# Kernel tuning notes

Measured on AMD Instinct MI355X. Metric: run time of the kernel, lower is better.

## Reference

```python
import jax, jax.numpy as jnp
import numpy as np

B, T, C, H = 128, 256, 384, 6
D = C // H  # head dim = 64


def setup_inputs() -> dict:
    key = jax.random.key(0)
    k1, k2, k3, k4, k5 = jax.random.split(key, 5)
    s = 0.02
    return {
        "x": jax.random.normal(k1, (B, T, C), dtype=jnp.float32),
        "W_qkv": jax.random.normal(k2, (C, 3 * C), dtype=jnp.float32) * s,
        "b_qkv": jax.random.normal(k3, (3 * C,), dtype=jnp.float32) * s,
        "W_proj": jax.random.normal(k4, (C, C), dtype=jnp.float32) * s,
        "b_proj": jax.random.normal(k5, (C,), dtype=jnp.float32) * s,
    }


def reference(x, W_qkv, b_qkv, W_proj, b_proj):
    Bv, Tv, Cv = x.shape
    # fused QKV projection, then split
    qkv = x @ W_qkv + b_qkv                      # [B,T,3C]
    q, k, v = jnp.split(qkv, 3, axis=-1)
    # [B,T,C] -> [B,H,T,D]
    q = q.reshape(Bv, Tv, H, D).transpose(0, 2, 1, 3)
    k = k.reshape(Bv, Tv, H, D).transpose(0, 2, 1, 3)
    v = v.reshape(Bv, Tv, H, D).transpose(0, 2, 1, 3)
    # causal masked scores, scaled by head_dim**-0.5
    scores = jnp.einsum("bhqd,bhkd->bhqk", q, k) * (D ** -0.5)
    causal = jnp.tril(jnp.ones((Tv, Tv), dtype=bool))
    scores = jnp.where(causal, scores, -jnp.inf)
    wt = jax.nn.softmax(scores, axis=-1)
    # dropout layers are identity in eval mode
    out = jnp.einsum("bhqk,bhkd->bhqd", wt, v)   # [B,H,T,D]
    out = out.transpose(0, 2, 1, 3).reshape(Bv, Tv, Cv)
    return out @ W_proj + b_proj
```

## Files before the change

### kernel.cpp

```cpp
#include <hip/hip_runtime.h>

typedef unsigned short u16;
typedef unsigned int u32;
typedef __attribute__((ext_vector_type(4))) float f32x4;
typedef __attribute__((ext_vector_type(8))) __bf16 bf16x8;
typedef __attribute__((ext_vector_type(2))) __bf16 bf16x2;

#define NEGINF (-1e30f)
#define QSCALE 0.18033688011112042f

__device__ __forceinline__ u16 f32_to_bf16(float f) {
  union { float f; unsigned int u; } v;
  v.f = f;
  unsigned int u = v.u;
  u += 0x7fffu + ((u >> 16) & 1u);
  return (u16)(u >> 16);
}

__device__ __forceinline__ u32 pk_bf16(float a, float b) {
  bf16x2 t;
  t.x = (__bf16)a;
  t.y = (__bf16)b;
  return __builtin_bit_cast(u32, t);
}

__device__ __forceinline__ f32x4 mfma_bf16(bf16x8 a, bf16x8 b, f32x4 c) {
  return __builtin_amdgcn_mfma_f32_16x16x32_bf16(a, b, c, 0, 0, 0);
}

#define GLOAD_LDS16(g, l) __builtin_amdgcn_global_load_lds( \
    (const __attribute__((address_space(1))) unsigned int*)(g), \
    (__attribute__((address_space(3))) unsigned int*)(l), 16, 0, 0)

__global__ void k_cvt4(const float4* __restrict__ in, u16* __restrict__ out, int nq) {
  int i = blockIdx.x * blockDim.x + threadIdx.x;
  if (i >= nq) return;
  float4 v = in[i];
  uint2 o;
  o.x = (unsigned int)f32_to_bf16(v.x) | ((unsigned int)f32_to_bf16(v.y) << 16);
  o.y = (unsigned int)f32_to_bf16(v.z) | ((unsigned int)f32_to_bf16(v.w) << 16);
  *(uint2*)(out + (size_t)i * 4) = o;
}

__global__ void k_tcvt(const float* __restrict__ in, u16* __restrict__ out, int K, int N) {
  int idx = blockIdx.x * blockDim.x + threadIdx.x;
  if (idx >= K * N) return;
  int k = idx / N, n = idx - k * N;
  out[(size_t)n * K + k] = f32_to_bf16(in[idx]);
}

__device__ __forceinline__ void gemm256x64(
    const u16* __restrict__ A, const u16* __restrict__ Bt,
    int mBase, int nBase, u16* lsA, u16* lsB,
    f32x4 acc[4][2], int lane, int wv, int wm, int wn) {
  const int l15 = lane & 15;
  size_t aoff[4];
  u32 aldso[4];
#pragma unroll
  for (int jj = 0; jj < 4; ++jj) {
    int c = wv * 256 + jj * 64 + lane;
    int row = c >> 3;
    int kc = (c & 7) ^ (row & 7);
    aoff[jj] = (size_t)(mBase + row) * 384 + kc * 8;
    aldso[jj] = (u32)(wv * 256 + jj * 64) * 8;
  }
  int cb = wv * 64 + lane;
  int brow = cb >> 3;
  size_t boff = (size_t)(nBase + brow) * 384 + (size_t)(((cb & 7) ^ (brow & 7)) * 8);
  u32 bldso = (u32)(wv * 64) * 8;

#define STAGE_T(kt, buf) do { \
  _Pragma("unroll") \
  for (int jj = 0; jj < 4; ++jj) \
    GLOAD_LDS16(A + aoff[jj] + (kt), lsA + (buf) * 16384 + aldso[jj]); \
  GLOAD_LDS16(Bt + boff + (kt), lsB + (buf) * 4096 + bldso); \
  } while (0)

  STAGE_T(0, 0);
#pragma unroll
  for (int t = 0; t < 6; ++t) {
    const int cur = t & 1;
    if (t < 5) {
      STAGE_T((t + 1) * 64, cur ^ 1);
      asm volatile("s_waitcnt vmcnt(5)" ::: "memory");
    } else {
      asm volatile("s_waitcnt vmcnt(0)" ::: "memory");
    }
    __builtin_amdgcn_s_barrier();
    const char* bA = (const char*)(lsA + cur * 16384);
    const char* bB = (const char*)(lsB + cur * 4096);
#pragma unroll
    for (int ks = 0; ks < 2; ++ks) {
      bf16x8 af[4], bfr[2];
#pragma unroll
      for (int i = 0; i < 4; ++i) {
        int row = wm * 64 + i * 16 + l15;
        af[i] = *(const bf16x8*)(bA + row * 128 + (((ks * 4 + (lane >> 4)) ^ (row & 7)) << 4));
      }
#pragma unroll
      for (int j = 0; j < 2; ++j) {
        int row = wn * 32 + j * 16 + l15;
        bfr[j] = *(const bf16x8*)(bB + row * 128 + (((ks * 4 + (lane >> 4)) ^ (row & 7)) << 4));
      }
#pragma unroll
      for (int i = 0; i < 4; ++i)
#pragma unroll
        for (int j = 0; j < 2; ++j)
          acc[i][j] = mfma_bf16(af[i], bfr[j], acc[i][j]);
    }
    __builtin_amdgcn_s_barrier();
  }
#undef STAGE_T
}

__global__ __launch_bounds__(512, 4) void k_qkv(
    const u16* __restrict__ A, const u16* __restrict__ Bt,
    const float* __restrict__ bias,
    u16* __restrict__ Qb, u16* __restrict__ Kb, u16* __restrict__ Vtb) {
  __shared__ __align__(16) u16 lsA[2 * 16384];
  __shared__ __align__(16) u16 lsB[2 * 4096];
  const int tid = threadIdx.x, lane = tid & 63, wv = tid >> 6;
  const int l15 = lane & 15, g = lane >> 4;
  const int wm = wv >> 1, wn = wv & 1;
  const int bid = (int)blockIdx.x;
  const int wgid = (bid & 7) * 288 + (bid >> 3);
  const int mtile = wgid / 18, ntile = wgid % 18;
  const int mBase = mtile * 256, nBase = ntile * 64;
  f32x4 acc[4][2] = {};
  gemm256x64(A, Bt, mBase, nBase, lsA, lsB, acc, lane, wv, wm, wn);

  const int part = nBase / 384;
  const int cbase = nBase - part * 384;
#pragma unroll
  for (int j = 0; j < 2; ++j) {
    int c = cbase + wn * 32 + j * 16 + l15;
    float bv = bias[nBase + wn * 32 + j * 16 + l15];
    int hh = c >> 6, d = c & 63;
    size_t bhh = (size_t)(mtile * 6 + hh);
#pragma unroll
    for (int i = 0; i < 4; ++i) {
      int t0 = wm * 64 + i * 16 + g * 4;
      if (part == 2) {
        uint2 w;
        w.x = pk_bf16(acc[i][j][0] + bv, acc[i][j][1] + bv);
        w.y = pk_bf16(acc[i][j][2] + bv, acc[i][j][3] + bv);
        *(uint2*)(Vtb + (bhh * 64 + d) * 256 + t0) = w;
      } else if (part == 0) {
#pragma unroll
        for (int r = 0; r < 4; ++r)
          Qb[(bhh * 256 + t0 + r) * 64 + d] = f32_to_bf16((acc[i][j][r] + bv) * QSCALE);
      } else {
#pragma unroll
        for (int r = 0; r < 4; ++r)
          Kb[(bhh * 256 + t0 + r) * 64 + d] = f32_to_bf16(acc[i][j][r] + bv);
      }
    }
  }
}

__global__ __launch_bounds__(64, 3) void k_attn(
    const u16* __restrict__ Qb, const u16* __restrict__ Kb,
    const u16* __restrict__ Vtb, u16* __restrict__ Ob) {
  __shared__ __align__(16) u16 lsP[32 * 64];
  const int lane = threadIdx.x;
  const int l15 = lane & 15, g = lane >> 4;
  const int s = 7 - (int)blockIdx.y;
  const int bh = blockIdx.x;
  const int b = bh / 6, h = bh % 6;
  const u16* Qh = Qb + (size_t)bh * (256 * 64);
  const u16* Kh = Kb + (size_t)bh * (256 * 64);
  const u16* Vh = Vtb + (size_t)bh * (64 * 256);
  const int ktiles = (s >> 1) + 1;
  char* pbuf = (char*)lsP;

  bf16x8 qf[2][2];
#pragma unroll
  for (int ks = 0; ks < 2; ++ks)
#pragma unroll
    for (int iq = 0; iq < 2; ++iq)
      qf[ks][iq] = *(const bf16x8*)(Qh + (size_t)(s * 32 + iq * 16 + l15) * 64 + ks * 32 + g * 8);

  f32x4 o[4][2] = {};
  float rl[2] = {0.f, 0.f};

#pragma unroll 1
  for (int kt = 0; kt < ktiles; ++kt) {
    bf16x8 kf[2][4];
#pragma unroll
    for (int ks = 0; ks < 2; ++ks)
#pragma unroll
      for (int jk = 0; jk < 4; ++jk)
        kf[ks][jk] = *(const bf16x8*)(Kh + (size_t)(kt * 64 + jk * 16 + l15) * 64 + ks * 32 + g * 8);

    f32x4 st[4][2] = {};
    __builtin_amdgcn_s_setprio(1);
#pragma unroll
    for (int ks = 0; ks < 2; ++ks)
#pragma unroll
      for (int jk = 0; jk < 4; ++jk)
#pragma unroll
        for (int iq = 0; iq < 2; ++iq)
          st[jk][iq] = mfma_bf16(kf[ks][jk], qf[ks][iq], st[jk][iq]);
    __builtin_amdgcn_s_setprio(0);

    bf16x8 vf[2][4];
#pragma unroll
    for (int ks = 0; ks < 2; ++ks)
#pragma unroll
      for (int jd = 0; jd < 4; ++jd)
        vf[ks][jd] = *(const bf16x8*)(Vh + (size_t)(jd * 16 + l15) * 256 + kt * 64 + ks * 32 + g * 8);

    if (kt == ktiles - 1) {
#pragma unroll
      for (int jk = 0; jk < 4; ++jk)
#pragma unroll
        for (int iq = 0; iq < 2; ++iq)
#pragma unroll
          for (int r = 0; r < 4; ++r)
            if (kt * 64 + jk * 16 + g * 4 + r > s * 32 + iq * 16 + l15)
              st[jk][iq][r] = NEGINF;
    }

    float rs[2] = {0.f, 0.f};
#pragma unroll
    for (int jk = 0; jk < 4; ++jk)
#pragma unroll
      for (int iq = 0; iq < 2; ++iq) {
        float p0 = __builtin_amdgcn_exp2f(st[jk][iq][0]);
        float p1 = __builtin_amdgcn_exp2f(st[jk][iq][1]);
        float p2 = __builtin_amdgcn_exp2f(st[jk][iq][2]);
        float p3 = __builtin_amdgcn_exp2f(st[jk][iq][3]);
        rs[iq] += (p0 + p1) + (p2 + p3);
        int q = iq * 16 + l15;
        int byte = (q * 128 + (jk * 16 + g * 4) * 2) ^ ((q & 7) << 4);
        uint2 w;
        w.x = pk_bf16(p0, p1);
        w.y = pk_bf16(p2, p3);
        *(uint2*)(pbuf + byte) = w;
      }
#pragma unroll
    for (int iq = 0; iq < 2; ++iq) {
      float v = rs[iq];
      v += __shfl_xor(v, 16);
      v += __shfl_xor(v, 32);
      rl[iq] += v;
    }

#pragma unroll
    for (int ks = 0; ks < 2; ++ks) {
      bf16x8 pf[2];
#pragma unroll
      for (int iq = 0; iq < 2; ++iq) {
        int q = iq * 16 + l15;
        pf[iq] = *(const bf16x8*)(pbuf + ((q * 128 + ks * 64 + g * 16) ^ ((q & 7) << 4)));
      }
      __builtin_amdgcn_s_setprio(1);
#pragma unroll
      for (int jd = 0; jd < 4; ++jd)
#pragma unroll
        for (int iq = 0; iq < 2; ++iq)
          o[jd][iq] = mfma_bf16(vf[ks][jd], pf[iq], o[jd][iq]);
      __builtin_amdgcn_s_setprio(0);
    }
  }

#pragma unroll
  for (int iq = 0; iq < 2; ++iq) {
    float inv = 1.0f / rl[iq];
    int q = iq * 16 + l15;
#pragma unroll
    for (int jd = 0; jd < 4; ++jd) {
      uint2 w;
      w.x = pk_bf16(o[jd][iq][0] * inv, o[jd][iq][1] * inv);
      w.y = pk_bf16(o[jd][iq][2] * inv, o[jd][iq][3] * inv);
      int byte = (q * 128 + jd * 32 + g * 8) ^ ((q & 7) << 4);
      *(uint2*)(pbuf + byte) = w;
    }
  }
  asm volatile("s_waitcnt lgkmcnt(0)" ::: "memory");
#pragma unroll
  for (int rep = 0; rep < 4; ++rep) {
    int row = rep * 8 + (lane >> 3);
    int c = lane & 7;
    uint4 v = *(const uint4*)(pbuf + row * 128 + ((c ^ (row & 7)) * 16));
    int t = s * 32 + row;
    *(uint4*)(Ob + ((size_t)(b * 256 + t)) * 384 + h * 64 + c * 8) = v;
  }
}

__global__ __launch_bounds__(512, 4) void k_proj(
    const u16* __restrict__ A, const u16* __restrict__ Bt,
    const float* __restrict__ bias, float* __restrict__ out) {
  __shared__ __align__(16) u16 lsA[2 * 16384];
  __shared__ __align__(16) u16 lsB[2 * 4096];
  const int tid = threadIdx.x, lane = tid & 63, wv = tid >> 6;
  const int l15 = lane & 15, g = lane >> 4;
  const int wm = wv >> 1, wn = wv & 1;
  const int bid = (int)blockIdx.x;
  const int wgid = (bid & 7) * 96 + (bid >> 3);
  const int mtile = wgid / 6, ntile = wgid % 6;
  const int mBase = mtile * 256, nBase = ntile * 64;
  f32x4 acc[4][2] = {};
  gemm256x64(A, Bt, mBase, nBase, lsA, lsB, acc, lane, wv, wm, wn);
#pragma unroll
  for (int j = 0; j < 2; ++j) {
    int col = nBase + wn * 32 + j * 16 + l15;
    float bv = bias[col];
#pragma unroll
    for (int i = 0; i < 4; ++i) {
      int m0 = mBase + wm * 64 + i * 16 + g * 4;
#pragma unroll
      for (int r = 0; r < 4; ++r)
        out[(size_t)(m0 + r) * 384 + col] = acc[i][j][r] + bv;
    }
  }
}

extern "C" void kernel_launch(void* const* d_in, const int* in_sizes, int n_in,
                              void* d_out, int out_size, void* d_ws, size_t ws_size,
                              hipStream_t stream) {
  const float* x     = (const float*)d_in[0];
  const float* Wqkv  = (const float*)d_in[1];
  const float* bqkv  = (const float*)d_in[2];
  const float* Wproj = (const float*)d_in[3];
  const float* bproj = (const float*)d_in[4];
  float* out = (float*)d_out;

  char* ws = (char*)d_ws;
  u16* xb     = (u16*)(ws);
  u16* wqkvb  = (u16*)(ws + 25165824);
  u16* wprojb = (u16*)(ws + 26050560);
  u16* Qb     = (u16*)(ws + 26345472);
  u16* Kb     = (u16*)(ws + 51511296);
  u16* Vtb    = (u16*)(ws + 76677120);
  u16* Ob     = (u16*)(ws + 101842944);

  k_cvt4<<<12288, 256, 0, stream>>>((const float4*)x, xb, 3145728);
  k_tcvt<<<1728, 256, 0, stream>>>(Wqkv, wqkvb, 384, 1152);
  k_tcvt<<<576, 256, 0, stream>>>(Wproj, wprojb, 384, 384);
  k_qkv<<<2304, 512, 0, stream>>>(xb, wqkvb, bqkv, Qb, Kb, Vtb);
  k_attn<<<dim3(768, 8), 64, 0, stream>>>(Qb, Kb, Vtb, Ob);
  k_proj<<<768, 512, 0, stream>>>(Ob, wprojb, bproj, out);
}
```

Baseline: 122.3 us.

## Swap MFMA operands for packed Q/K stores and retile proj GEMM to 128x128

In the QKV kernel, the Q and K tiles now run the GEMM with MFMA operands swapped, so each lane holds four consecutive head-dim values. The epilogue can then write packed 8-byte stores instead of scattered 2-byte ones. The output projection moves from 256x64 tiles with 512 threads to 128x128 square tiles with 256 threads. It uses a simpler single-buffered LDS loop with raised priority around the MFMAs, which gives better operand reuse per tile but drops the double-buffer overlap.

```diff
diff --git a/kernel.cpp b/kernel.cpp
--- a/kernel.cpp
+++ b/kernel.cpp
@@ -49,6 +49,7 @@
   out[(size_t)n * K + k] = f32_to_bf16(in[idx]);
 }
 
+template <bool SW>
 __device__ __forceinline__ void gemm256x64(
     const u16* __restrict__ A, const u16* __restrict__ Bt,
     int mBase, int nBase, u16* lsA, u16* lsB,
@@ -106,7 +107,8 @@
       for (int i = 0; i < 4; ++i)
 #pragma unroll
         for (int j = 0; j < 2; ++j)
-          acc[i][j] = mfma_bf16(af[i], bfr[j], acc[i][j]);
+          acc[i][j] = SW ? mfma_bf16(bfr[j], af[i], acc[i][j])
+                         : mfma_bf16(af[i], bfr[j], acc[i][j]);
     }
     __builtin_amdgcn_s_barrier();
   }
@@ -126,33 +128,43 @@
   const int wgid = (bid & 7) * 288 + (bid >> 3);
   const int mtile = wgid / 18, ntile = wgid % 18;
   const int mBase = mtile * 256, nBase = ntile * 64;
+  const int part = ntile / 6;
+  const int hh = ntile % 6;
+
   f32x4 acc[4][2] = {};
-  gemm256x64(A, Bt, mBase, nBase, lsA, lsB, acc, lane, wv, wm, wn);
-
-  const int part = nBase / 384;
-  const int cbase = nBase - part * 384;
-#pragma unroll
-  for (int j = 0; j < 2; ++j) {
-    int c = cbase + wn * 32 + j * 16 + l15;
-    float bv = bias[nBase + wn * 32 + j * 16 + l15];
-    int hh = c >> 6, d = c & 63;
-    size_t bhh = (size_t)(mtile * 6 + hh);
-#pragma unroll
-    for (int i = 0; i < 4; ++i) {
-      int t0 = wm * 64 + i * 16 + g * 4;
-      if (part == 2) {
+  if (part == 2) {
+    gemm256x64<false>(A, Bt, mBase, nBase, lsA, lsB, acc, lane, wv, wm, wn);
+#pragma unroll
+    for (int j = 0; j < 2; ++j) {
+      int d = wn * 32 + j * 16 + l15;
+      float bv = bias[nBase + wn * 32 + j * 16 + l15];
+#pragma unroll
+      for (int i = 0; i < 4; ++i) {
+        int t0 = wm * 64 + i * 16 + g * 4;
+        size_t bhh = (size_t)(mtile * 6 + hh);
         uint2 w;
         w.x = pk_bf16(acc[i][j][0] + bv, acc[i][j][1] + bv);
         w.y = pk_bf16(acc[i][j][2] + bv, acc[i][j][3] + bv);
         *(uint2*)(Vtb + (bhh * 64 + d) * 256 + t0) = w;
-      } else if (part == 0) {
-#pragma unroll
-        for (int r = 0; r < 4; ++r)
-          Qb[(bhh * 256 + t0 + r) * 64 + d] = f32_to_bf16((acc[i][j][r] + bv) * QSCALE);
-      } else {
-#pragma unroll
-        for (int r = 0; r < 4; ++r)
-          Kb[(bhh * 256 + t0 + r) * 64 + d] = f32_to_bf16(acc[i][j][r] + bv);
+      }
+    }
+  } else {
+    gemm256x64<true>(A, Bt, mBase, nBase, lsA, lsB, acc, lane, wv, wm, wn);
+    u16* dst = (part == 0) ? Qb : Kb;
+    const float scale = (part == 0) ? QSCALE : 1.0f;
+#pragma unroll
+    for (int j = 0; j < 2; ++j) {
+      int dbase = wn * 32 + j * 16 + g * 4;
+      float4 bv4 = *(const float4*)(bias + nBase + dbase);
+#pragma unroll
+      for (int i = 0; i < 4; ++i) {
+        int t = mBase + wm * 64 + i * 16 + l15;
+        int bb = t >> 8, tt = t & 255;
+        size_t bhh = (size_t)(bb * 6 + hh);
+        uint2 w;
+        w.x = pk_bf16((acc[i][j][0] + bv4.x) * scale, (acc[i][j][1] + bv4.y) * scale);
+        w.y = pk_bf16((acc[i][j][2] + bv4.z) * scale, (acc[i][j][3] + bv4.w) * scale);
+        *(uint2*)(dst + (bhh * 256 + tt) * 64 + dbase) = w;
       }
     }
   }
@@ -288,23 +300,72 @@
   }
 }
 
-__global__ __launch_bounds__(512, 4) void k_proj(
+__device__ __forceinline__ void gemm128sq(
+    const u16* __restrict__ A, const u16* __restrict__ Bt,
+    int mBase, int nBase, u16* lsA, u16* lsB,
+    f32x4 acc[4][4], int lane, int wv) {
+  const int l15 = lane & 15, g = lane >> 4;
+  const int wm = wv >> 1, wn = wv & 1;
+  size_t aoff[4], boff[4];
+  u32 ldso[4];
+#pragma unroll
+  for (int jj = 0; jj < 4; ++jj) {
+    int c = jj * 256 + wv * 64 + lane;
+    int row = c >> 3;
+    int kc = (c & 7) ^ (row & 7);
+    aoff[jj] = (size_t)(mBase + row) * 384 + kc * 8;
+    boff[jj] = (size_t)(nBase + row) * 384 + kc * 8;
+    ldso[jj] = (u32)c * 8;
+  }
+#pragma unroll 1
+  for (int t = 0; t < 6; ++t) {
+#pragma unroll
+    for (int jj = 0; jj < 4; ++jj) {
+      GLOAD_LDS16(A + aoff[jj] + t * 64, lsA + ldso[jj]);
+      GLOAD_LDS16(Bt + boff[jj] + t * 64, lsB + ldso[jj]);
+    }
+    __syncthreads();
+#pragma unroll
+    for (int ks = 0; ks < 2; ++ks) {
+      bf16x8 af[4], bfr[4];
+#pragma unroll
+      for (int i = 0; i < 4; ++i) {
+        int row = wm * 64 + i * 16 + l15;
+        af[i] = *(const bf16x8*)((const char*)lsA + row * 128 + (((ks * 4 + g) ^ (row & 7)) << 4));
+      }
+#pragma unroll
+      for (int j = 0; j < 4; ++j) {
+        int row = wn * 64 + j * 16 + l15;
+        bfr[j] = *(const bf16x8*)((const char*)lsB + row * 128 + (((ks * 4 + g) ^ (row & 7)) << 4));
+      }
+      __builtin_amdgcn_s_setprio(1);
+#pragma unroll
+      for (int i = 0; i < 4; ++i)
+#pragma unroll
+        for (int j = 0; j < 4; ++j)
+          acc[i][j] = mfma_bf16(af[i], bfr[j], acc[i][j]);
+      __builtin_amdgcn_s_setprio(0);
+    }
+    __syncthreads();
+  }
+}
+
+__global__ __launch_bounds__(256, 3) void k_proj(
     const u16* __restrict__ A, const u16* __restrict__ Bt,
     const float* __restrict__ bias, float* __restrict__ out) {
-  __shared__ __align__(16) u16 lsA[2 * 16384];
-  __shared__ __align__(16) u16 lsB[2 * 4096];
+  __shared__ __align__(16) u16 lsA[8192];
+  __shared__ __align__(16) u16 lsB[8192];
   const int tid = threadIdx.x, lane = tid & 63, wv = tid >> 6;
   const int l15 = lane & 15, g = lane >> 4;
   const int wm = wv >> 1, wn = wv & 1;
   const int bid = (int)blockIdx.x;
   const int wgid = (bid & 7) * 96 + (bid >> 3);
-  const int mtile = wgid / 6, ntile = wgid % 6;
-  const int mBase = mtile * 256, nBase = ntile * 64;
-  f32x4 acc[4][2] = {};
-  gemm256x64(A, Bt, mBase, nBase, lsA, lsB, acc, lane, wv, wm, wn);
-#pragma unroll
-  for (int j = 0; j < 2; ++j) {
-    int col = nBase + wn * 32 + j * 16 + l15;
+  const int mBase = (wgid / 3) * 128, nBase = (wgid % 3) * 128;
+  f32x4 acc[4][4] = {};
+  gemm128sq(A, Bt, mBase, nBase, lsA, lsB, acc, lane, wv);
+#pragma unroll
+  for (int j = 0; j < 4; ++j) {
+    int col = nBase + wn * 64 + j * 16 + l15;
     float bv = bias[col];
 #pragma unroll
     for (int i = 0; i < 4; ++i) {
@@ -340,5 +401,5 @@
   k_tcvt<<<576, 256, 0, stream>>>(Wproj, wprojb, 384, 384);
   k_qkv<<<2304, 512, 0, stream>>>(xb, wqkvb, bqkv, Qb, Kb, Vtb);
   k_attn<<<dim3(768, 8), 64, 0, stream>>>(Qb, Kb, Vtb, Ob);
-  k_proj<<<768, 512, 0, stream>>>(Ob, wprojb, bproj, out);
-}
+  k_proj<<<768, 256, 0, stream>>>(Ob, wprojb, bproj, out);
+}
```

Result: slower. 135.2 us (+10.5%).
